# Performance work log

Measured on AMD Instinct MI355X. Metric: run time of the kernel, lower is better.

## Reference

```python
import jax, jax.numpy as jnp
import numpy as np

T = 20000          # document length in tokens
EMBED_DIM = 300    # GloVe 840B.300d
STATE_DIM = 400    # 2 * lstm_dim (bidirectional)
HIDDEN = 150       # Scorer hidden_dim default
MAX_N = 10         # span widths 1..10
G_DIM = 2 * STATE_DIM + EMBED_DIM  # 1100


def _mlp3(x, W1, b1, W2, b2, W3, b3):
    # Scorer: Linear -> ReLU -> Linear -> ReLU -> Linear(->1)
    h = jax.nn.relu(x @ W1 + b1)
    h = jax.nn.relu(h @ W2 + b2)
    return h @ W3 + b3


def _span_features(embeds, states, attn_logits):
    """Vectorized SpanEncoder: for every window of width n in 1..MAX_N,
    softmax the per-token attention logits within the window, attention-pool
    the word embeddings, and concat [state_start, state_end, pooled].
    Returns g of shape [sum_n (T-n+1), G_DIM]."""
    gs = []
    for n in range(1, MAX_N + 1):
        S = T - n + 1  # number of width-n spans
        # [n, S] windowed logits and [n, S, E] windowed embeds via shifted slices
        a = jnp.stack([attn_logits[j:j + S] for j in range(n)], axis=0)
        w = jax.nn.softmax(a, axis=0)  # softmax within each span (dim=0 in torch)
        we = jnp.stack([embeds[j:j + S] for j in range(n)], axis=0)
        pooled = jnp.einsum('ns,nse->se', w, we)  # [S, E]
        g = jnp.concatenate([states[:S], states[n - 1:n - 1 + S], pooled], axis=-1)
        gs.append(g)
    return jnp.concatenate(gs, axis=0)


def setup_inputs() -> dict:
    key = jax.random.key(0)
    ks = jax.random.split(key, 16)
    sc = 0.05
    return {
        'embeds': jax.random.normal(ks[0], (T, EMBED_DIM), jnp.float32),
        'states': jax.random.normal(ks[1], (T, STATE_DIM), jnp.float32),
        'attn_W1': jax.random.normal(ks[2], (STATE_DIM, HIDDEN), jnp.float32) * sc,
        'attn_b1': jnp.zeros((HIDDEN,), jnp.float32),
        'attn_W2': jax.random.normal(ks[3], (HIDDEN, HIDDEN), jnp.float32) * sc,
        'attn_b2': jnp.zeros((HIDDEN,), jnp.float32),
        'attn_W3': jax.random.normal(ks[4], (HIDDEN, 1), jnp.float32) * sc,
        'attn_b3': jnp.zeros((1,), jnp.float32),
        'sc_W1': jax.random.normal(ks[5], (G_DIM, HIDDEN), jnp.float32) * sc,
        'sc_b1': jnp.zeros((HIDDEN,), jnp.float32),
        'sc_W2': jax.random.normal(ks[6], (HIDDEN, HIDDEN), jnp.float32) * sc,
        'sc_b2': jnp.zeros((HIDDEN,), jnp.float32),
        'sc_W3': jax.random.normal(ks[7], (HIDDEN, 1), jnp.float32) * sc,
        'sc_b3': jnp.zeros((1,), jnp.float32),
    }


def reference(embeds, states, attn_W1, attn_b1, attn_W2, attn_b2, attn_W3, attn_b3,
              sc_W1, sc_b1, sc_W2, sc_b2, sc_W3, sc_b3):
    # SpanAttention: per-token scalar attention logit from the BiLSTM state
    attn_logits = _mlp3(states, attn_W1, attn_b1, attn_W2, attn_b2, attn_W3, attn_b3)[:, 0]
    # SpanEncoder: ragged windowed attention pooling + boundary-state concat
    g = _span_features(embeds, states, attn_logits)  # [10T-45, 1100]
    # SpanScorer: MLP score per span
    scores = _mlp3(g, sc_W1, sc_b1, sc_W2, sc_b2, sc_W3, sc_b3)[:, 0]
    return scores
```

## Files before the change

### kernel.cpp

```cpp
#include <hip/hip_runtime.h>
#include <hip/hip_bf16.h>
#include <math.h>

#define T_LEN 20000
#define HID 150

typedef __attribute__((ext_vector_type(8))) __bf16 bf16x8;
typedef __attribute__((ext_vector_type(4))) float f32x4;

__device__ __forceinline__ short f2bf(float f) {
    unsigned u = __float_as_uint(f);
    u = (u + 0x7fff + ((u >> 16) & 1)) >> 16;
    return (short)u;
}

__device__ __forceinline__ unsigned pk2(float a, float b) {
    __hip_bfloat162 h = __float22bfloat162_rn(make_float2(a, b));
    return *(unsigned*)&h;
}

__device__ __forceinline__ bf16x8 cvt8(float4 a, float4 b) {
    union { unsigned u[4]; bf16x8 v; } r;
    r.u[0] = pk2(a.x, a.y);
    r.u[1] = pk2(a.z, a.w);
    r.u[2] = pk2(b.x, b.y);
    r.u[3] = pk2(b.z, b.w);
    return r.v;
}

__device__ __forceinline__ float2 ubf2(unsigned u) {
    return make_float2(__uint_as_float(u << 16),
                       __uint_as_float(u & 0xffff0000u));
}

__global__ __launch_bounds__(256) void wprep(
    const float* __restrict__ sc_W1, const float* __restrict__ attn_W1,
    const float* __restrict__ attn_W2, const float* __restrict__ sc_W2,
    short* __restrict__ wbf)
{
    int t = blockIdx.x * 256 + threadIdx.x;
    if (t >= 318720) return;
    float v = 0.f;
    if (t < 133120) {
        int y = t / 66560, r = t - y * 66560;
        int nn = r / 416, k = r - nn * 416;
        if (nn < HID && k < 400) v = sc_W1[(long)(y * 400 + k) * HID + nn];
    } else if (t < 199680) {
        int r = t - 133120;
        int nn = r / 416, k = r - nn * 416;
        if (nn < HID && k < 400) v = attn_W1[(long)k * HID + nn];
    } else if (t < 266240) {
        int r = t - 199680;
        int nn = r / 416, k = r - nn * 416;
        if (nn < HID && k < 300) v = sc_W1[(long)(800 + k) * HID + nn];
    } else if (t < 291840) {
        int r = t - 266240;
        int nn = r / 160, k = r - nn * 160;
        if (nn < HID && k < HID) v = attn_W2[(long)k * HID + nn];
    } else {
        int r = t - 291840;
        int nn = r / 168, k = r - nn * 168;
        if (nn < HID && k < HID) v = sc_W2[(long)k * HID + nn];
    }
    wbf[t] = f2bf(v);
}

__global__ __launch_bounds__(256) void fusedA(
    const float* __restrict__ states, const short* __restrict__ wbf,
    const float* __restrict__ scb1, const float* __restrict__ ab1,
    const float* __restrict__ ab2, const float* __restrict__ aW3,
    const float* __restrict__ ab3,
    short* __restrict__ Ubf, short* __restrict__ Vbf, float* __restrict__ logits)
{
    __shared__ short h1s[16 * 168];
    __shared__ float red[16][4];
    __shared__ float sb1[160], ab1s[160];
    const int tid = threadIdx.x;
    const int w = tid >> 6, lane = tid & 63;
    const int ml = lane & 15, kg = lane >> 4;
    const int m0 = blockIdx.x * 16;

    for (int t = tid; t < 160; t += 256) {
        sb1[t]  = (t < HID) ? scb1[t] : 0.f;
        ab1s[t] = (t < HID) ? ab1[t]  : 0.f;
    }
    __syncthreads();

    const float* Arow = states + (long)(m0 + ml) * 400;
    const int nT = (w < 2) ? 8 : 7;

    f32x4 acc[8];
    #pragma unroll
    for (int t = 0; t < 8; ++t) acc[t] = (f32x4){0.f, 0.f, 0.f, 0.f};

    for (int ks = 0; ks < 13; ++ks) {
        int k = ks * 32 + kg * 8;
        float4 a0 = make_float4(0.f, 0.f, 0.f, 0.f);
        float4 a1 = make_float4(0.f, 0.f, 0.f, 0.f);
        if (k + 4 <= 400) a0 = *(const float4*)&Arow[k];
        if (k + 8 <= 400) a1 = *(const float4*)&Arow[k + 4];
        bf16x8 af = cvt8(a0, a1);
        #pragma unroll
        for (int t = 0; t < 8; ++t) {
            if (t < nT) {
                int nt = 4 * t + w;
                bf16x8 bf = *(const bf16x8*)&wbf[(long)(nt * 16 + ml) * 416 + k];
                acc[t] = __builtin_amdgcn_mfma_f32_16x16x32_bf16(bf, af, acc[t], 0, 0, 0);
            }
        }
    }

    #pragma unroll
    for (int t = 0; t < 8; ++t) {
        if (t < nT) {
            int nt = 4 * t + w;
            if (nt < 10) {
                int col0 = nt * 16 + kg * 4;
                float v[4];
                #pragma unroll
                for (int r = 0; r < 4; ++r) {
                    int c = col0 + r;
                    v[r] = (c < HID) ? acc[t][r] + sb1[c] : 0.f;
                }
                *(uint2*)&Ubf[(long)(m0 + ml) * 160 + col0] =
                    make_uint2(pk2(v[0], v[1]), pk2(v[2], v[3]));
            } else if (nt < 20) {
                int col0 = (nt - 10) * 16 + kg * 4;
                float v[4];
                #pragma unroll
                for (int r = 0; r < 4; ++r) {
                    int c = col0 + r;
                    v[r] = (c < HID) ? acc[t][r] : 0.f;
                }
                *(uint2*)&Vbf[(long)(m0 + ml) * 160 + col0] =
                    make_uint2(pk2(v[0], v[1]), pk2(v[2], v[3]));
            } else {
                int col0 = (nt - 20) * 16 + kg * 4;
                float v[4];
                #pragma unroll
                for (int r = 0; r < 4; ++r) {
                    int c = col0 + r;
                    v[r] = (c < HID) ? fmaxf(acc[t][r] + ab1s[c], 0.f) : 0.f;
                }
                *(uint2*)&h1s[ml * 168 + col0] =
                    make_uint2(pk2(v[0], v[1]), pk2(v[2], v[3]));
            }
        }
    }
    __syncthreads();

    const short* At2 = wbf + 266240;
    bf16x8 af2[5];
    #pragma unroll
    for (int ks = 0; ks < 5; ++ks)
        af2[ks] = *(const bf16x8*)&h1s[ml * 168 + ks * 32 + kg * 8];

    const int nT2 = (w < 2) ? 3 : 2;
    float score[4] = {0.f, 0.f, 0.f, 0.f};
    #pragma unroll
    for (int t = 0; t < 3; ++t) {
        if (t < nT2) {
            int nt = 4 * t + w;
            f32x4 a2 = {0.f, 0.f, 0.f, 0.f};
            #pragma unroll
            for (int ks = 0; ks < 5; ++ks) {
                bf16x8 bf = *(const bf16x8*)&At2[(long)(nt * 16 + ml) * 160 + ks * 32 + kg * 8];
                a2 = __builtin_amdgcn_mfma_f32_16x16x32_bf16(af2[ks], bf, a2, 0, 0, 0);
            }
            int col = nt * 16 + ml;
            float b2v = (col < HID) ? ab2[col] : 0.f;
            float w3v = (col < HID) ? aW3[col] : 0.f;
            #pragma unroll
            for (int r = 0; r < 4; ++r)
                score[r] += fmaxf(a2[r] + b2v, 0.f) * w3v;
        }
    }
    #pragma unroll
    for (int r = 0; r < 4; ++r) {
        score[r] += __shfl_xor(score[r], 1);
        score[r] += __shfl_xor(score[r], 2);
        score[r] += __shfl_xor(score[r], 4);
        score[r] += __shfl_xor(score[r], 8);
    }
    if (ml == 0) {
        #pragma unroll
        for (int r = 0; r < 4; ++r) red[kg * 4 + r][w] = score[r];
    }
    __syncthreads();
    if (tid < 16)
        logits[m0 + tid] = red[tid][0] + red[tid][1] + red[tid][2] + red[tid][3] + ab3[0];
}

__global__ __launch_bounds__(256) void pkern(
    const float* __restrict__ embeds, const short* __restrict__ wbf,
    short* __restrict__ Pbf)
{
    const int tid = threadIdx.x;
    const int w = tid >> 6, lane = tid & 63;
    const int ml = lane & 15, kg = lane >> 4;
    const int m0 = blockIdx.x * 16;
    const short* Bt = wbf + 199680;

    const float* Arow = embeds + (long)(m0 + ml) * 300;
    const int nT = (w < 2) ? 3 : 2;

    f32x4 acc[3];
    #pragma unroll
    for (int t = 0; t < 3; ++t) acc[t] = (f32x4){0.f, 0.f, 0.f, 0.f};

    for (int ks = 0; ks < 10; ++ks) {
        int k = ks * 32 + kg * 8;
        float4 a0 = make_float4(0.f, 0.f, 0.f, 0.f);
        float4 a1 = make_float4(0.f, 0.f, 0.f, 0.f);
        if (k + 4 <= 300) a0 = *(const float4*)&Arow[k];
        if (k + 8 <= 300) a1 = *(const float4*)&Arow[k + 4];
        bf16x8 af = cvt8(a0, a1);
        #pragma unroll
        for (int t = 0; t < 3; ++t) {
            if (t < nT) {
                int nt = 4 * t + w;
                bf16x8 bf = *(const bf16x8*)&Bt[(long)(nt * 16 + ml) * 416 + k];
                acc[t] = __builtin_amdgcn_mfma_f32_16x16x32_bf16(bf, af, acc[t], 0, 0, 0);
            }
        }
    }

    #pragma unroll
    for (int t = 0; t < 3; ++t) {
        if (t < nT) {
            int nt = 4 * t + w;
            int col0 = nt * 16 + kg * 4;
            float v[4];
            #pragma unroll
            for (int r = 0; r < 4; ++r) {
                int c = col0 + r;
                v[r] = (c < HID) ? acc[t][r] : 0.f;
            }
            *(uint2*)&Pbf[(long)(m0 + ml) * 160 + col0] =
                make_uint2(pk2(v[0], v[1]), pk2(v[2], v[3]));
        }
    }
}

__global__ __launch_bounds__(256) void span_all(
    const short* __restrict__ Ubf, const short* __restrict__ Vbf,
    const short* __restrict__ Pbf, const float* __restrict__ logits,
    const short* __restrict__ W2t, const float* __restrict__ b2,
    const float* __restrict__ W3, const float* __restrict__ b3,
    float* __restrict__ out)
{
    __shared__ short h1s[32 * 168];
    __shared__ float Ls[48], ebuf[48];
    __shared__ float b2s[160], W3s[160];
    __shared__ float red[32][2];

    const int tid = threadIdx.x;
    const int s0 = blockIdx.x * 32;

    if (tid < 48) {
        int r = s0 + tid; if (r > T_LEN - 1) r = T_LEN - 1;
        Ls[tid] = (tid < 41) ? logits[r] : -1e30f;
    }
    for (int t = tid; t < 160; t += 256) {
        b2s[t] = (t < HID) ? b2[t] : 0.f;
        W3s[t] = (t < HID) ? W3[t] : 0.f;
    }
    __syncthreads();
    if (tid < 48) {
        float M = -1e30f;
        for (int t = 0; t < 41; ++t) M = fmaxf(M, Ls[t]);
        ebuf[tid] = (tid < 41) ? expf(Ls[tid] - M) : 0.f;
    }
    __syncthreads();

    const int i = tid >> 3;
    const int q = tid & 7;
    const int d0 = 20 * q;
    const int s = s0 + i;
    int su = s; if (su > T_LEN - 1) su = T_LEN - 1;

    float Ur[20];
    {
        const uint2* U2 = (const uint2*)&Ubf[(long)su * 160 + d0];
        #pragma unroll
        for (int c = 0; c < 5; ++c) {
            uint2 uv = U2[c];
            float2 a = ubf2(uv.x), b_ = ubf2(uv.y);
            Ur[4 * c + 0] = a.x;  Ur[4 * c + 1] = a.y;
            Ur[4 * c + 2] = b_.x; Ur[4 * c + 3] = b_.y;
        }
    }
    float accp[20];
    #pragma unroll
    for (int d = 0; d < 20; ++d) accp[d] = 0.f;
    float den = 0.f;

    const int w = tid >> 6, lane = tid & 63;
    const int ml = lane & 15, kg = lane >> 4;
    const int mt = w >> 1;
    const int nt0 = (w & 1) * 5;
    const float bb = b3[0];

    for (int n = 1; n <= 10; ++n) {
        int rr_ = s + n - 1; if (rr_ > T_LEN - 1) rr_ = T_LEN - 1;
        float e = ebuf[i + n - 1];
        den += e;
        {
            const uint2* P2 = (const uint2*)&Pbf[(long)rr_ * 160 + d0];
            #pragma unroll
            for (int c = 0; c < 5; ++c) {
                uint2 pv = P2[c];
                float2 a = ubf2(pv.x), b_ = ubf2(pv.y);
                accp[4 * c + 0] += e * a.x;  accp[4 * c + 1] += e * a.y;
                accp[4 * c + 2] += e * b_.x; accp[4 * c + 3] += e * b_.y;
            }
        }
        float invd = 1.f / den;
        {
            const uint2* V2 = (const uint2*)&Vbf[(long)rr_ * 160 + d0];
            #pragma unroll
            for (int c = 0; c < 5; ++c) {
                uint2 vv = V2[c];
                float2 a = ubf2(vv.x), b_ = ubf2(vv.y);
                float x0 = fmaxf(Ur[4 * c + 0] + a.x  + accp[4 * c + 0] * invd, 0.f);
                float x1 = fmaxf(Ur[4 * c + 1] + a.y  + accp[4 * c + 1] * invd, 0.f);
                float x2 = fmaxf(Ur[4 * c + 2] + b_.x + accp[4 * c + 2] * invd, 0.f);
                float x3 = fmaxf(Ur[4 * c + 3] + b_.y + accp[4 * c + 3] * invd, 0.f);
                *(uint2*)&h1s[i * 168 + d0 + 4 * c] =
                    make_uint2(pk2(x0, x1), pk2(x2, x3));
            }
        }
        __syncthreads();

        bf16x8 af[5];
        #pragma unroll
        for (int ks = 0; ks < 5; ++ks)
            af[ks] = *(const bf16x8*)&h1s[(mt * 16 + ml) * 168 + ks * 32 + kg * 8];

        float sc[4] = {0.f, 0.f, 0.f, 0.f};
        #pragma unroll
        for (int j = 0; j < 5; ++j) {
            int nt = nt0 + j;
            f32x4 a2 = {0.f, 0.f, 0.f, 0.f};
            #pragma unroll
            for (int ks = 0; ks < 5; ++ks) {
                bf16x8 bf = *(const bf16x8*)&W2t[(long)(nt * 16 + ml) * 168 + ks * 32 + kg * 8];
                a2 = __builtin_amdgcn_mfma_f32_16x16x32_bf16(af[ks], bf, a2, 0, 0, 0);
            }
            int col = nt * 16 + ml;
            float b2v = b2s[col], w3v = W3s[col];
            #pragma unroll
            for (int r = 0; r < 4; ++r)
                sc[r] += fmaxf(a2[r] + b2v, 0.f) * w3v;
        }
        #pragma unroll
        for (int r = 0; r < 4; ++r) {
            sc[r] += __shfl_xor(sc[r], 1);
            sc[r] += __shfl_xor(sc[r], 2);
            sc[r] += __shfl_xor(sc[r], 4);
            sc[r] += __shfl_xor(sc[r], 8);
        }
        if (ml == 0) {
            #pragma unroll
            for (int r = 0; r < 4; ++r)
                red[mt * 16 + kg * 4 + r][w & 1] = sc[r];
        }
        __syncthreads();
        if (tid < 32) {
            int S = T_LEN - n + 1;
            int off = (n - 1) * (T_LEN + 1) - (n - 1) * n / 2;
            int sr = s0 + tid;
            if (sr < S) out[off + sr] = red[tid][0] + red[tid][1] + bb;
        }
        __syncthreads();
    }
}

extern "C" void kernel_launch(void* const* d_in, const int* in_sizes, int n_in,
                              void* d_out, int out_size, void* d_ws, size_t ws_size,
                              hipStream_t stream) {
    const float* embeds  = (const float*)d_in[0];
    const float* states  = (const float*)d_in[1];
    const float* attn_W1 = (const float*)d_in[2];
    const float* attn_b1 = (const float*)d_in[3];
    const float* attn_W2 = (const float*)d_in[4];
    const float* attn_b2 = (const float*)d_in[5];
    const float* attn_W3 = (const float*)d_in[6];
    const float* attn_b3 = (const float*)d_in[7];
    const float* sc_W1   = (const float*)d_in[8];
    const float* sc_b1   = (const float*)d_in[9];
    const float* sc_W2   = (const float*)d_in[10];
    const float* sc_b2   = (const float*)d_in[11];
    const float* sc_W3   = (const float*)d_in[12];
    const float* sc_b3   = (const float*)d_in[13];
    float* out = (float*)d_out;

    short* wsS = (short*)d_ws;
    short* Ubf = wsS;
    short* Vbf = wsS + 3200256;
    short* Pbf = wsS + 6400512;
    short* wbf = wsS + 9600768;
    float* logits = (float*)(wsS + 9920000);

    wprep<<<1245, 256, 0, stream>>>(sc_W1, attn_W1, attn_W2, sc_W2, wbf);
    fusedA<<<1250, 256, 0, stream>>>(states, wbf, sc_b1, attn_b1,
                                     attn_b2, attn_W3, attn_b3,
                                     Ubf, Vbf, logits);
    pkern<<<1250, 256, 0, stream>>>(embeds, wbf, Pbf);
    span_all<<<625, 256, 0, stream>>>(Ubf, Vbf, Pbf, logits,
                                      wbf + 291840, sc_b2, sc_W3, sc_b3,
                                      out);
}
```

Baseline: 220.9 us.

## Pre-swizzle weights into MFMA fragment order and process 32 rows per block

```diff
diff --git a/kernel.cpp b/kernel.cpp
--- a/kernel.cpp
+++ b/kernel.cpp
@@ -36,49 +36,64 @@
 __global__ __launch_bounds__(256) void wprep(
     const float* __restrict__ sc_W1, const float* __restrict__ attn_W1,
     const float* __restrict__ attn_W2, const float* __restrict__ sc_W2,
-    short* __restrict__ wbf)
+    short* __restrict__ frag)
 {
     int t = blockIdx.x * 256 + threadIdx.x;
-    if (t >= 318720) return;
+    if (t >= 302080) return;
     float v = 0.f;
-    if (t < 133120) {
-        int y = t / 66560, r = t - y * 66560;
-        int nn = r / 416, k = r - nn * 416;
-        if (nn < HID && k < 400) v = sc_W1[(long)(y * 400 + k) * HID + nn];
-    } else if (t < 199680) {
-        int r = t - 133120;
-        int nn = r / 416, k = r - nn * 416;
-        if (nn < HID && k < 400) v = attn_W1[(long)k * HID + nn];
-    } else if (t < 266240) {
+    if (t < 199680) {
+        int e = t & 7, g = t >> 3;
+        int lane = g & 63, h = g >> 6;
+        int ks = h % 13, nt = h / 13;
+        int k = ks * 32 + (lane >> 4) * 8 + e;
+        int cs = (nt % 10) * 16 + (lane & 15);
+        if (k < 400 && cs < HID) {
+            if (nt < 10)      v = sc_W1[(long)k * HID + cs];
+            else if (nt < 20) v = sc_W1[(long)(400 + k) * HID + cs];
+            else              v = attn_W1[(long)k * HID + cs];
+        }
+    } else if (t < 250880) {
         int r = t - 199680;
-        int nn = r / 416, k = r - nn * 416;
-        if (nn < HID && k < 300) v = sc_W1[(long)(800 + k) * HID + nn];
-    } else if (t < 291840) {
-        int r = t - 266240;
-        int nn = r / 160, k = r - nn * 160;
-        if (nn < HID && k < HID) v = attn_W2[(long)k * HID + nn];
+        int e = r & 7, g = r >> 3;
+        int lane = g & 63, h = g >> 6;
+        int ks = h % 10, nt = h / 10;
+        int k = ks * 32 + (lane >> 4) * 8 + e;
+        int cs = nt * 16 + (lane & 15);
+        if (k < 300 && cs < HID) v = sc_W1[(long)(800 + k) * HID + cs];
+    } else if (t < 276480) {
+        int r = t - 250880;
+        int e = r & 7, g = r >> 3;
+        int lane = g & 63, h = g >> 6;
+        int ks = h % 5, nt = h / 5;
+        int k = ks * 32 + (lane >> 4) * 8 + e;
+        int cs = nt * 16 + (lane & 15);
+        if (k < HID && cs < HID) v = attn_W2[(long)k * HID + cs];
     } else {
-        int r = t - 291840;
-        int nn = r / 168, k = r - nn * 168;
-        if (nn < HID && k < HID) v = sc_W2[(long)k * HID + nn];
-    }
-    wbf[t] = f2bf(v);
+        int r = t - 276480;
+        int e = r & 7, g = r >> 3;
+        int lane = g & 63, h = g >> 6;
+        int ks = h % 5, nt = h / 5;
+        int k = ks * 32 + (lane >> 4) * 8 + e;
+        int cs = nt * 16 + (lane & 15);
+        if (k < HID && cs < HID) v = sc_W2[(long)k * HID + cs];
+    }
+    frag[t] = f2bf(v);
 }
 
 __global__ __launch_bounds__(256) void fusedA(
-    const float* __restrict__ states, const short* __restrict__ wbf,
+    const float* __restrict__ states, const short* __restrict__ frag,
     const float* __restrict__ scb1, const float* __restrict__ ab1,
     const float* __restrict__ ab2, const float* __restrict__ aW3,
     const float* __restrict__ ab3,
     short* __restrict__ Ubf, short* __restrict__ Vbf, float* __restrict__ logits)
 {
-    __shared__ short h1s[16 * 168];
-    __shared__ float red[16][4];
+    __shared__ short h1s[32 * 168];
+    __shared__ float red[32][4];
     __shared__ float sb1[160], ab1s[160];
     const int tid = threadIdx.x;
     const int w = tid >> 6, lane = tid & 63;
     const int ml = lane & 15, kg = lane >> 4;
-    const int m0 = blockIdx.x * 16;
+    const int m0 = blockIdx.x * 32;
 
     for (int t = tid; t < 160; t += 256) {
         sb1[t]  = (t < HID) ? scb1[t] : 0.f;
@@ -86,26 +101,31 @@
     }
     __syncthreads();
 
-    const float* Arow = states + (long)(m0 + ml) * 400;
+    const float* Arow0 = states + (long)(m0 + ml) * 400;
+    const float* Arow1 = states + (long)(m0 + 16 + ml) * 400;
     const int nT = (w < 2) ? 8 : 7;
 
-    f32x4 acc[8];
-    #pragma unroll
-    for (int t = 0; t < 8; ++t) acc[t] = (f32x4){0.f, 0.f, 0.f, 0.f};
+    f32x4 acc0[8], acc1[8];
+    #pragma unroll
+    for (int t = 0; t < 8; ++t) {
+        acc0[t] = (f32x4){0.f, 0.f, 0.f, 0.f};
+        acc1[t] = (f32x4){0.f, 0.f, 0.f, 0.f};
+    }
 
     for (int ks = 0; ks < 13; ++ks) {
         int k = ks * 32 + kg * 8;
-        float4 a0 = make_float4(0.f, 0.f, 0.f, 0.f);
-        float4 a1 = make_float4(0.f, 0.f, 0.f, 0.f);
-        if (k + 4 <= 400) a0 = *(const float4*)&Arow[k];
-        if (k + 8 <= 400) a1 = *(const float4*)&Arow[k + 4];
-        bf16x8 af = cvt8(a0, a1);
+        float4 a0 = make_float4(0.f, 0.f, 0.f, 0.f), a1 = a0, b0 = a0, b1 = a0;
+        if (k + 4 <= 400) { a0 = *(const float4*)&Arow0[k]; b0 = *(const float4*)&Arow1[k]; }
+        if (k + 8 <= 400) { a1 = *(const float4*)&Arow0[k + 4]; b1 = *(const float4*)&Arow1[k + 4]; }
+        bf16x8 af0 = cvt8(a0, a1);
+        bf16x8 af1 = cvt8(b0, b1);
         #pragma unroll
         for (int t = 0; t < 8; ++t) {
             if (t < nT) {
                 int nt = 4 * t + w;
-                bf16x8 bf = *(const bf16x8*)&wbf[(long)(nt * 16 + ml) * 416 + k];
-                acc[t] = __builtin_amdgcn_mfma_f32_16x16x32_bf16(bf, af, acc[t], 0, 0, 0);
+                bf16x8 bf = *(const bf16x8*)&frag[(long)(((nt * 13 + ks) << 6) | lane) << 3];
+                acc0[t] = __builtin_amdgcn_mfma_f32_16x16x32_bf16(bf, af0, acc0[t], 0, 0, 0);
+                acc1[t] = __builtin_amdgcn_mfma_f32_16x16x32_bf16(bf, af1, acc1[t], 0, 0, 0);
             }
         }
     }
@@ -116,111 +136,133 @@
             int nt = 4 * t + w;
             if (nt < 10) {
                 int col0 = nt * 16 + kg * 4;
-                float v[4];
+                float v0[4], v1[4];
                 #pragma unroll
                 for (int r = 0; r < 4; ++r) {
                     int c = col0 + r;
-                    v[r] = (c < HID) ? acc[t][r] + sb1[c] : 0.f;
+                    v0[r] = (c < HID) ? acc0[t][r] + sb1[c] : 0.f;
+                    v1[r] = (c < HID) ? acc1[t][r] + sb1[c] : 0.f;
                 }
                 *(uint2*)&Ubf[(long)(m0 + ml) * 160 + col0] =
-                    make_uint2(pk2(v[0], v[1]), pk2(v[2], v[3]));
+                    make_uint2(pk2(v0[0], v0[1]), pk2(v0[2], v0[3]));
+                *(uint2*)&Ubf[(long)(m0 + 16 + ml) * 160 + col0] =
+                    make_uint2(pk2(v1[0], v1[1]), pk2(v1[2], v1[3]));
             } else if (nt < 20) {
                 int col0 = (nt - 10) * 16 + kg * 4;
-                float v[4];
+                float v0[4], v1[4];
                 #pragma unroll
                 for (int r = 0; r < 4; ++r) {
                     int c = col0 + r;
-                    v[r] = (c < HID) ? acc[t][r] : 0.f;
+                    v0[r] = (c < HID) ? acc0[t][r] : 0.f;
+                    v1[r] = (c < HID) ? acc1[t][r] : 0.f;
                 }
                 *(uint2*)&Vbf[(long)(m0 + ml) * 160 + col0] =
-                    make_uint2(pk2(v[0], v[1]), pk2(v[2], v[3]));
+                    make_uint2(pk2(v0[0], v0[1]), pk2(v0[2], v0[3]));
+                *(uint2*)&Vbf[(long)(m0 + 16 + ml) * 160 + col0] =
+                    make_uint2(pk2(v1[0], v1[1]), pk2(v1[2], v1[3]));
             } else {
                 int col0 = (nt - 20) * 16 + kg * 4;
-                float v[4];
+                float v0[4], v1[4];
                 #pragma unroll
                 for (int r = 0; r < 4; ++r) {
                     int c = col0 + r;
-                    v[r] = (c < HID) ? fmaxf(acc[t][r] + ab1s[c], 0.f) : 0.f;
+                    v0[r] = (c < HID) ? fmaxf(acc0[t][r] + ab1s[c], 0.f) : 0.f;
+                    v1[r] = (c < HID) ? fmaxf(acc1[t][r] + ab1s[c], 0.f) : 0.f;
                 }
                 *(uint2*)&h1s[ml * 168 + col0] =
-                    make_uint2(pk2(v[0], v[1]), pk2(v[2], v[3]));
+                    make_uint2(pk2(v0[0], v0[1]), pk2(v0[2], v0[3]));
+                *(uint2*)&h1s[(16 + ml) * 168 + col0] =
+                    make_uint2(pk2(v1[0], v1[1]), pk2(v1[2], v1[3]));
             }
         }
     }
     __syncthreads();
 
-    const short* At2 = wbf + 266240;
-    bf16x8 af2[5];
-    #pragma unroll
-    for (int ks = 0; ks < 5; ++ks)
-        af2[ks] = *(const bf16x8*)&h1s[ml * 168 + ks * 32 + kg * 8];
+    const short* fAt2 = frag + 250880;
+    bf16x8 af2a[5], af2b[5];
+    #pragma unroll
+    for (int ks = 0; ks < 5; ++ks) {
+        af2a[ks] = *(const bf16x8*)&h1s[ml * 168 + ks * 32 + kg * 8];
+        af2b[ks] = *(const bf16x8*)&h1s[(16 + ml) * 168 + ks * 32 + kg * 8];
+    }
 
     const int nT2 = (w < 2) ? 3 : 2;
-    float score[4] = {0.f, 0.f, 0.f, 0.f};
+    float sca[4] = {0.f, 0.f, 0.f, 0.f}, scb[4] = {0.f, 0.f, 0.f, 0.f};
     #pragma unroll
     for (int t = 0; t < 3; ++t) {
         if (t < nT2) {
             int nt = 4 * t + w;
-            f32x4 a2 = {0.f, 0.f, 0.f, 0.f};
+            f32x4 a2 = {0.f, 0.f, 0.f, 0.f}, b2_ = {0.f, 0.f, 0.f, 0.f};
             #pragma unroll
             for (int ks = 0; ks < 5; ++ks) {
-                bf16x8 bf = *(const bf16x8*)&At2[(long)(nt * 16 + ml) * 160 + ks * 32 + kg * 8];
-                a2 = __builtin_amdgcn_mfma_f32_16x16x32_bf16(af2[ks], bf, a2, 0, 0, 0);
+                bf16x8 bf = *(const bf16x8*)&fAt2[(long)(((nt * 5 + ks) << 6) | lane) << 3];
+                a2  = __builtin_amdgcn_mfma_f32_16x16x32_bf16(af2a[ks], bf, a2, 0, 0, 0);
+                b2_ = __builtin_amdgcn_mfma_f32_16x16x32_bf16(af2b[ks], bf, b2_, 0, 0, 0);
             }
             int col = nt * 16 + ml;
             float b2v = (col < HID) ? ab2[col] : 0.f;
             float w3v = (col < HID) ? aW3[col] : 0.f;
             #pragma unroll
-            for (int r = 0; r < 4; ++r)
-                score[r] += fmaxf(a2[r] + b2v, 0.f) * w3v;
+            for (int r = 0; r < 4; ++r) {
+                sca[r] += fmaxf(a2[r] + b2v, 0.f) * w3v;
+                scb[r] += fmaxf(b2_[r] + b2v, 0.f) * w3v;
+            }
         }
     }
     #pragma unroll
     for (int r = 0; r < 4; ++r) {
-        score[r] += __shfl_xor(score[r], 1);
-        score[r] += __shfl_xor(score[r], 2);
-        score[r] += __shfl_xor(score[r], 4);
-        score[r] += __shfl_xor(score[r], 8);
+        sca[r] += __shfl_xor(sca[r], 1); scb[r] += __shfl_xor(scb[r], 1);
+        sca[r] += __shfl_xor(sca[r], 2); scb[r] += __shfl_xor(scb[r], 2);
+        sca[r] += __shfl_xor(sca[r], 4); scb[r] += __shfl_xor(scb[r], 4);
+        sca[r] += __shfl_xor(sca[r], 8); scb[r] += __shfl_xor(scb[r], 8);
     }
     if (ml == 0) {
         #pragma unroll
-        for (int r = 0; r < 4; ++r) red[kg * 4 + r][w] = score[r];
+        for (int r = 0; r < 4; ++r) {
+            red[kg * 4 + r][w] = sca[r];
+            red[16 + kg * 4 + r][w] = scb[r];
+        }
     }
     __syncthreads();
-    if (tid < 16)
+    if (tid < 32)
         logits[m0 + tid] = red[tid][0] + red[tid][1] + red[tid][2] + red[tid][3] + ab3[0];
 }
 
 __global__ __launch_bounds__(256) void pkern(
-    const float* __restrict__ embeds, const short* __restrict__ wbf,
+    const float* __restrict__ embeds, const short* __restrict__ frag,
     short* __restrict__ Pbf)
 {
     const int tid = threadIdx.x;
     const int w = tid >> 6, lane = tid & 63;
     const int ml = lane & 15, kg = lane >> 4;
-    const int m0 = blockIdx.x * 16;
-    const short* Bt = wbf + 199680;
-
-    const float* Arow = embeds + (long)(m0 + ml) * 300;
+    const int m0 = blockIdx.x * 32;
+    const short* fP = frag + 199680;
+
+    const float* Arow0 = embeds + (long)(m0 + ml) * 300;
+    const float* Arow1 = embeds + (long)(m0 + 16 + ml) * 300;
     const int nT = (w < 2) ? 3 : 2;
 
-    f32x4 acc[3];
-    #pragma unroll
-    for (int t = 0; t < 3; ++t) acc[t] = (f32x4){0.f, 0.f, 0.f, 0.f};
+    f32x4 acc0[3], acc1[3];
+    #pragma unroll
+    for (int t = 0; t < 3; ++t) {
+        acc0[t] = (f32x4){0.f, 0.f, 0.f, 0.f};
+        acc1[t] = (f32x4){0.f, 0.f, 0.f, 0.f};
+    }
 
     for (int ks = 0; ks < 10; ++ks) {
         int k = ks * 32 + kg * 8;
-        float4 a0 = make_float4(0.f, 0.f, 0.f, 0.f);
-        float4 a1 = make_float4(0.f, 0.f, 0.f, 0.f);
-        if (k + 4 <= 300) a0 = *(const float4*)&Arow[k];
-        if (k + 8 <= 300) a1 = *(const float4*)&Arow[k + 4];
-        bf16x8 af = cvt8(a0, a1);
+        float4 a0 = make_float4(0.f, 0.f, 0.f, 0.f), a1 = a0, b0 = a0, b1 = a0;
+        if (k + 4 <= 300) { a0 = *(const float4*)&Arow0[k]; b0 = *(const float4*)&Arow1[k]; }
+        if (k + 8 <= 300) { a1 = *(const float4*)&Arow0[k + 4]; b1 = *(const float4*)&Arow1[k + 4]; }
+        bf16x8 af0 = cvt8(a0, a1);
+        bf16x8 af1 = cvt8(b0, b1);
         #pragma unroll
         for (int t = 0; t < 3; ++t) {
             if (t < nT) {
                 int nt = 4 * t + w;
-                bf16x8 bf = *(const bf16x8*)&Bt[(long)(nt * 16 + ml) * 416 + k];
-                acc[t] = __builtin_amdgcn_mfma_f32_16x16x32_bf16(bf, af, acc[t], 0, 0, 0);
+                bf16x8 bf = *(const bf16x8*)&fP[(long)(((nt * 10 + ks) << 6) | lane) << 3];
+                acc0[t] = __builtin_amdgcn_mfma_f32_16x16x32_bf16(bf, af0, acc0[t], 0, 0, 0);
+                acc1[t] = __builtin_amdgcn_mfma_f32_16x16x32_bf16(bf, af1, acc1[t], 0, 0, 0);
             }
         }
     }
@@ -230,14 +272,17 @@
         if (t < nT) {
             int nt = 4 * t + w;
             int col0 = nt * 16 + kg * 4;
-            float v[4];
+            float v0[4], v1[4];
             #pragma unroll
             for (int r = 0; r < 4; ++r) {
                 int c = col0 + r;
-                v[r] = (c < HID) ? acc[t][r] : 0.f;
+                v0[r] = (c < HID) ? acc0[t][r] : 0.f;
+                v1[r] = (c < HID) ? acc1[t][r] : 0.f;
             }
             *(uint2*)&Pbf[(long)(m0 + ml) * 160 + col0] =
-                make_uint2(pk2(v[0], v[1]), pk2(v[2], v[3]));
+                make_uint2(pk2(v0[0], v0[1]), pk2(v0[2], v0[3]));
+            *(uint2*)&Pbf[(long)(m0 + 16 + ml) * 160 + col0] =
+                make_uint2(pk2(v1[0], v1[1]), pk2(v1[2], v1[3]));
         }
     }
 }
@@ -245,7 +290,7 @@
 __global__ __launch_bounds__(256) void span_all(
     const short* __restrict__ Ubf, const short* __restrict__ Vbf,
     const short* __restrict__ Pbf, const float* __restrict__ logits,
-    const short* __restrict__ W2t, const float* __restrict__ b2,
+    const short* __restrict__ fW2, const float* __restrict__ b2,
     const float* __restrict__ W3, const float* __restrict__ b3,
     float* __restrict__ out)
 {
@@ -344,7 +389,7 @@
             f32x4 a2 = {0.f, 0.f, 0.f, 0.f};
             #pragma unroll
             for (int ks = 0; ks < 5; ++ks) {
-                bf16x8 bf = *(const bf16x8*)&W2t[(long)(nt * 16 + ml) * 168 + ks * 32 + kg * 8];
+                bf16x8 bf = *(const bf16x8*)&fW2[(long)(((nt * 5 + ks) << 6) | lane) << 3];
                 a2 = __builtin_amdgcn_mfma_f32_16x16x32_bf16(af[ks], bf, a2, 0, 0, 0);
             }
             int col = nt * 16 + ml;
@@ -399,15 +444,15 @@
     short* Ubf = wsS;
     short* Vbf = wsS + 3200256;
     short* Pbf = wsS + 6400512;
-    short* wbf = wsS + 9600768;
-    float* logits = (float*)(wsS + 9920000);
-
-    wprep<<<1245, 256, 0, stream>>>(sc_W1, attn_W1, attn_W2, sc_W2, wbf);
-    fusedA<<<1250, 256, 0, stream>>>(states, wbf, sc_b1, attn_b1,
-                                     attn_b2, attn_W3, attn_b3,
-                                     Ubf, Vbf, logits);
-    pkern<<<1250, 256, 0, stream>>>(embeds, wbf, Pbf);
+    short* frag = wsS + 9600768;
+    float* logits = (float*)(wsS + 9902848);
+
+    wprep<<<1180, 256, 0, stream>>>(sc_W1, attn_W1, attn_W2, sc_W2, frag);
+    fusedA<<<625, 256, 0, stream>>>(states, frag, sc_b1, attn_b1,
+                                    attn_b2, attn_W3, attn_b3,
+                                    Ubf, Vbf, logits);
+    pkern<<<625, 256, 0, stream>>>(embeds, frag, Pbf);
     span_all<<<625, 256, 0, stream>>>(Ubf, Vbf, Pbf, logits,
-                                      wbf + 291840, sc_b2, sc_W3, sc_b3,
+                                      frag + 276480, sc_b2, sc_W3, sc_b3,
                                       out);
 }
```

Result: faster. 216.5 us (-2.0%).

## Pre-swizzle weights into MFMA fragment order and split span widths across blocks

Applied to the files above, without the earlier changes.

```diff
diff --git a/kernel.cpp b/kernel.cpp
--- a/kernel.cpp
+++ b/kernel.cpp
@@ -36,37 +36,52 @@
 __global__ __launch_bounds__(256) void wprep(
     const float* __restrict__ sc_W1, const float* __restrict__ attn_W1,
     const float* __restrict__ attn_W2, const float* __restrict__ sc_W2,
-    short* __restrict__ wbf)
+    short* __restrict__ frag)
 {
     int t = blockIdx.x * 256 + threadIdx.x;
-    if (t >= 318720) return;
+    if (t >= 302080) return;
     float v = 0.f;
-    if (t < 133120) {
-        int y = t / 66560, r = t - y * 66560;
-        int nn = r / 416, k = r - nn * 416;
-        if (nn < HID && k < 400) v = sc_W1[(long)(y * 400 + k) * HID + nn];
-    } else if (t < 199680) {
-        int r = t - 133120;
-        int nn = r / 416, k = r - nn * 416;
-        if (nn < HID && k < 400) v = attn_W1[(long)k * HID + nn];
-    } else if (t < 266240) {
+    if (t < 199680) {
+        int e = t & 7, g = t >> 3;
+        int lane = g & 63, h = g >> 6;
+        int ks = h % 13, nt = h / 13;
+        int k = ks * 32 + (lane >> 4) * 8 + e;
+        int cs = (nt % 10) * 16 + (lane & 15);
+        if (k < 400 && cs < HID) {
+            if (nt < 10)      v = sc_W1[(long)k * HID + cs];
+            else if (nt < 20) v = sc_W1[(long)(400 + k) * HID + cs];
+            else              v = attn_W1[(long)k * HID + cs];
+        }
+    } else if (t < 250880) {
         int r = t - 199680;
-        int nn = r / 416, k = r - nn * 416;
-        if (nn < HID && k < 300) v = sc_W1[(long)(800 + k) * HID + nn];
-    } else if (t < 291840) {
-        int r = t - 266240;
-        int nn = r / 160, k = r - nn * 160;
-        if (nn < HID && k < HID) v = attn_W2[(long)k * HID + nn];
+        int e = r & 7, g = r >> 3;
+        int lane = g & 63, h = g >> 6;
+        int ks = h % 10, nt = h / 10;
+        int k = ks * 32 + (lane >> 4) * 8 + e;
+        int cs = nt * 16 + (lane & 15);
+        if (k < 300 && cs < HID) v = sc_W1[(long)(800 + k) * HID + cs];
+    } else if (t < 276480) {
+        int r = t - 250880;
+        int e = r & 7, g = r >> 3;
+        int lane = g & 63, h = g >> 6;
+        int ks = h % 5, nt = h / 5;
+        int k = ks * 32 + (lane >> 4) * 8 + e;
+        int cs = nt * 16 + (lane & 15);
+        if (k < HID && cs < HID) v = attn_W2[(long)k * HID + cs];
     } else {
-        int r = t - 291840;
-        int nn = r / 168, k = r - nn * 168;
-        if (nn < HID && k < HID) v = sc_W2[(long)k * HID + nn];
-    }
-    wbf[t] = f2bf(v);
+        int r = t - 276480;
+        int e = r & 7, g = r >> 3;
+        int lane = g & 63, h = g >> 6;
+        int ks = h % 5, nt = h / 5;
+        int k = ks * 32 + (lane >> 4) * 8 + e;
+        int cs = nt * 16 + (lane & 15);
+        if (k < HID && cs < HID) v = sc_W2[(long)k * HID + cs];
+    }
+    frag[t] = f2bf(v);
 }
 
 __global__ __launch_bounds__(256) void fusedA(
-    const float* __restrict__ states, const short* __restrict__ wbf,
+    const float* __restrict__ states, const short* __restrict__ frag,
     const float* __restrict__ scb1, const float* __restrict__ ab1,
     const float* __restrict__ ab2, const float* __restrict__ aW3,
     const float* __restrict__ ab3,
@@ -104,7 +119,7 @@
         for (int t = 0; t < 8; ++t) {
             if (t < nT) {
                 int nt = 4 * t + w;
-                bf16x8 bf = *(const bf16x8*)&wbf[(long)(nt * 16 + ml) * 416 + k];
+                bf16x8 bf = *(const bf16x8*)&frag[(long)(((nt * 13 + ks) << 6) | lane) << 3];
                 acc[t] = __builtin_amdgcn_mfma_f32_16x16x32_bf16(bf, af, acc[t], 0, 0, 0);
             }
         }
@@ -149,7 +164,7 @@
     }
     __syncthreads();
 
-    const short* At2 = wbf + 266240;
+    const short* fAt2 = frag + 250880;
     bf16x8 af2[5];
     #pragma unroll
     for (int ks = 0; ks < 5; ++ks)
@@ -164,7 +179,7 @@
             f32x4 a2 = {0.f, 0.f, 0.f, 0.f};
             #pragma unroll
             for (int ks = 0; ks < 5; ++ks) {
-                bf16x8 bf = *(const bf16x8*)&At2[(long)(nt * 16 + ml) * 160 + ks * 32 + kg * 8];
+                bf16x8 bf = *(const bf16x8*)&fAt2[(long)(((nt * 5 + ks) << 6) | lane) << 3];
                 a2 = __builtin_amdgcn_mfma_f32_16x16x32_bf16(af2[ks], bf, a2, 0, 0, 0);
             }
             int col = nt * 16 + ml;
@@ -192,14 +207,14 @@
 }
 
 __global__ __launch_bounds__(256) void pkern(
-    const float* __restrict__ embeds, const short* __restrict__ wbf,
+    const float* __restrict__ embeds, const short* __restrict__ frag,
     short* __restrict__ Pbf)
 {
     const int tid = threadIdx.x;
     const int w = tid >> 6, lane = tid & 63;
     const int ml = lane & 15, kg = lane >> 4;
     const int m0 = blockIdx.x * 16;
-    const short* Bt = wbf + 199680;
+    const short* fP = frag + 199680;
 
     const float* Arow = embeds + (long)(m0 + ml) * 300;
     const int nT = (w < 2) ? 3 : 2;
@@ -219,7 +234,7 @@
         for (int t = 0; t < 3; ++t) {
             if (t < nT) {
                 int nt = 4 * t + w;
-                bf16x8 bf = *(const bf16x8*)&Bt[(long)(nt * 16 + ml) * 416 + k];
+                bf16x8 bf = *(const bf16x8*)&fP[(long)(((nt * 10 + ks) << 6) | lane) << 3];
                 acc[t] = __builtin_amdgcn_mfma_f32_16x16x32_bf16(bf, af, acc[t], 0, 0, 0);
             }
         }
@@ -245,7 +260,7 @@
 __global__ __launch_bounds__(256) void span_all(
     const short* __restrict__ Ubf, const short* __restrict__ Vbf,
     const short* __restrict__ Pbf, const float* __restrict__ logits,
-    const short* __restrict__ W2t, const float* __restrict__ b2,
+    const short* __restrict__ fW2, const float* __restrict__ b2,
     const float* __restrict__ W3, const float* __restrict__ b3,
     float* __restrict__ out)
 {
@@ -256,6 +271,8 @@
 
     const int tid = threadIdx.x;
     const int s0 = blockIdx.x * 32;
+    const int nlo = blockIdx.y ? 6 : 1;
+    const int nhi = blockIdx.y ? 10 : 5;
 
     if (tid < 48) {
         int r = s0 + tid; if (r > T_LEN - 1) r = T_LEN - 1;
@@ -295,13 +312,27 @@
     for (int d = 0; d < 20; ++d) accp[d] = 0.f;
     float den = 0.f;
 
+    for (int j = 0; j < nlo - 1; ++j) {
+        int rr_ = s + j; if (rr_ > T_LEN - 1) rr_ = T_LEN - 1;
+        float e = ebuf[i + j];
+        den += e;
+        const uint2* P2 = (const uint2*)&Pbf[(long)rr_ * 160 + d0];
+        #pragma unroll
+        for (int c = 0; c < 5; ++c) {
+            uint2 pv = P2[c];
+            float2 a = ubf2(pv.x), b_ = ubf2(pv.y);
+            accp[4 * c + 0] += e * a.x;  accp[4 * c + 1] += e * a.y;
+            accp[4 * c + 2] += e * b_.x; accp[4 * c + 3] += e * b_.y;
+        }
+    }
+
     const int w = tid >> 6, lane = tid & 63;
     const int ml = lane & 15, kg = lane >> 4;
     const int mt = w >> 1;
     const int nt0 = (w & 1) * 5;
     const float bb = b3[0];
 
-    for (int n = 1; n <= 10; ++n) {
+    for (int n = nlo; n <= nhi; ++n) {
         int rr_ = s + n - 1; if (rr_ > T_LEN - 1) rr_ = T_LEN - 1;
         float e = ebuf[i + n - 1];
         den += e;
@@ -344,7 +375,7 @@
             f32x4 a2 = {0.f, 0.f, 0.f, 0.f};
             #pragma unroll
             for (int ks = 0; ks < 5; ++ks) {
-                bf16x8 bf = *(const bf16x8*)&W2t[(long)(nt * 16 + ml) * 168 + ks * 32 + kg * 8];
+                bf16x8 bf = *(const bf16x8*)&fW2[(long)(((nt * 5 + ks) << 6) | lane) << 3];
                 a2 = __builtin_amdgcn_mfma_f32_16x16x32_bf16(af[ks], bf, a2, 0, 0, 0);
             }
             int col = nt * 16 + ml;
@@ -399,15 +430,15 @@
     short* Ubf = wsS;
     short* Vbf = wsS + 3200256;
     short* Pbf = wsS + 6400512;
-    short* wbf = wsS + 9600768;
-    float* logits = (float*)(wsS + 9920000);
-
-    wprep<<<1245, 256, 0, stream>>>(sc_W1, attn_W1, attn_W2, sc_W2, wbf);
-    fusedA<<<1250, 256, 0, stream>>>(states, wbf, sc_b1, attn_b1,
+    short* frag = wsS + 9600768;
+    float* logits = (float*)(wsS + 9902848);
+
+    wprep<<<1180, 256, 0, stream>>>(sc_W1, attn_W1, attn_W2, sc_W2, frag);
+    fusedA<<<1250, 256, 0, stream>>>(states, frag, sc_b1, attn_b1,
                                      attn_b2, attn_W3, attn_b3,
                                      Ubf, Vbf, logits);
-    pkern<<<1250, 256, 0, stream>>>(embeds, wbf, Pbf);
-    span_all<<<625, 256, 0, stream>>>(Ubf, Vbf, Pbf, logits,
-                                      wbf + 291840, sc_b2, sc_W3, sc_b3,
-                                      out);
-}
+    pkern<<<1250, 256, 0, stream>>>(embeds, frag, Pbf);
+    span_all<<<dim3(625, 2), 256, 0, stream>>>(Ubf, Vbf, Pbf, logits,
+                                               frag + 276480, sc_b2, sc_W3, sc_b3,
+                                               out);
+}
```

Result: faster. 200.0 us (-9.5%).
